# Kernel tuning notes

Measured on AMD Instinct MI355X. Metric: run time of the kernel, lower is better.

## Reference

```python
import jax, jax.numpy as jnp
import numpy as np

H = 128          # hidden_dim
L = 10           # num_iterations
NC = 8000        # check nodes
NV = 16000       # var nodes
E = 60000        # edges per direction
INPUT_SCALE = 0.1
LN_EPS = 1e-6


def _glorot(key, shape):
    fan_in, fan_out = shape[0], shape[-1]
    lim = np.sqrt(6.0 / (fan_in + fan_out))
    return jax.random.uniform(key, shape, jnp.float32, -lim, lim)


def _ln(x, g, b):
    m = jnp.mean(x, axis=-1, keepdims=True)
    v = jnp.var(x, axis=-1, keepdims=True)
    return g * (x - m) / jnp.sqrt(v + LN_EPS) + b


def _gru(x, h, W, U, b):
    # Keras GRUCell, reset_after=True; gate order: z (update), r (reset), h (candidate)
    xa = x @ W + b[0]            # [N, 3H]
    ha = h @ U + b[1]            # [N, 3H]
    z = jax.nn.sigmoid(xa[:, :H] + ha[:, :H])
    r = jax.nn.sigmoid(xa[:, H:2 * H] + ha[:, H:2 * H])
    hh = jnp.tanh(xa[:, 2 * H:] + r * ha[:, 2 * H:])
    return z * h + (1.0 - z) * hh


def setup_inputs() -> dict:
    key = jax.random.key(0)
    ks = jax.random.split(key, 24)
    d = {
        'check_feats': jax.random.normal(ks[0], (NC, 1), jnp.float32),
        'var_feats': jax.random.normal(ks[1], (NV, 1), jnp.float32),
        'c2v_src': jax.random.randint(ks[2], (E,), 0, NC, jnp.int32),
        'c2v_tgt': jax.random.randint(ks[3], (E,), 0, NV, jnp.int32),
        'v2c_src': jax.random.randint(ks[4], (E,), 0, NV, jnp.int32),
        'v2c_tgt': jax.random.randint(ks[5], (E,), 0, NC, jnp.int32),
        # input transforms (Dense 1->H) + LayerNorm params
        'Wc_in': _glorot(ks[6], (1, H)), 'bc_in': jnp.zeros((H,), jnp.float32),
        'Wv_in': _glorot(ks[7], (1, H)), 'bv_in': jnp.zeros((H,), jnp.float32),
        'gc_ln': jnp.ones((H,), jnp.float32), 'bc_ln': jnp.zeros((H,), jnp.float32),
        'gv_ln': jnp.ones((H,), jnp.float32), 'bv_ln': jnp.zeros((H,), jnp.float32),
        # SimpleConv message Dense(2H->H) per receiving node set
        'Wmsg_c': _glorot(ks[8], (2 * H, H)), 'bmsg_c': jnp.zeros((H,), jnp.float32),
        'Wmsg_v': _glorot(ks[9], (2 * H, H)), 'bmsg_v': jnp.zeros((H,), jnp.float32),
        # NextStateFromConcat Dense(2H->H)
        'Wns_c': _glorot(ks[10], (2 * H, H)), 'bns_c': jnp.zeros((H,), jnp.float32),
        'Wns_v': _glorot(ks[11], (2 * H, H)), 'bns_v': jnp.zeros((H,), jnp.float32),
        # GRU cells: kernel [H,3H], recurrent [H,3H], bias [2,3H]
        'Wg_c': _glorot(ks[12], (H, 3 * H)), 'Ug_c': _glorot(ks[13], (H, 3 * H)),
        'bg_c': jnp.zeros((2, 3 * H), jnp.float32),
        'Wg_v': _glorot(ks[14], (H, 3 * H)), 'Ug_v': _glorot(ks[15], (H, 3 * H)),
        'bg_v': jnp.zeros((2, 3 * H), jnp.float32),
        # final predictor Dense(H->1), bias = logit(p_error)
        'Wf': _glorot(ks[16], (H, 1)),
        'bf': jnp.full((1,), np.log((4.0 / NV) / (1 - 4.0 / NV)), jnp.float32),
    }
    return d


def reference(check_feats, var_feats, c2v_src, c2v_tgt, v2c_src, v2c_tgt,
              Wc_in, bc_in, Wv_in, bv_in, gc_ln, bc_ln, gv_ln, bv_ln,
              Wmsg_c, bmsg_c, Wmsg_v, bmsg_v, Wns_c, bns_c, Wns_v, bns_v,
              Wg_c, Ug_c, bg_c, Wg_v, Ug_v, bg_v, Wf, bf):
    hc = _ln((INPUT_SCALE * check_feats) @ Wc_in + bc_in, gc_ln, bc_ln)  # [NC,H]
    hv = _ln((INPUT_SCALE * var_feats) @ Wv_in + bv_in, gv_ln, bv_ln)    # [NV,H]
    for _ in range(L):
        # v_to_c SimpleConv: concat(sender var state, receiver check state) -> Dense+ELU -> scatter-sum
        m_vc = jax.nn.elu(jnp.concatenate([hv[v2c_src], hc[v2c_tgt]], axis=-1) @ Wmsg_c + bmsg_c)
        agg_c = jax.ops.segment_sum(m_vc, v2c_tgt, num_segments=NC)
        # c_to_v SimpleConv
        m_cv = jax.nn.elu(jnp.concatenate([hc[c2v_src], hv[c2v_tgt]], axis=-1) @ Wmsg_v + bmsg_v)
        agg_v = jnp.asarray(jax.ops.segment_sum(m_cv, c2v_tgt, num_segments=NV))
        # NextStateFromConcat: Dense(concat(old_state, pooled)) + ELU
        upd_c = jax.nn.elu(jnp.concatenate([hc, agg_c], axis=-1) @ Wns_c + bns_c)
        upd_v = jax.nn.elu(jnp.concatenate([hv, agg_v], axis=-1) @ Wns_v + bns_v)
        # GRU state update (update info is the input, prev state is the hidden state)
        hc = _gru(upd_c, hc, Wg_c, Ug_c, bg_c)
        hv = _gru(upd_v, hv, Wg_v, Ug_v, bg_v)
    # dropout is identity at inference; final Dense(H->1), squeeze
    return (hv @ Wf + bf)[:, 0]
```

## Files before the change

kernel.cpp:

```cpp
#include <hip/hip_runtime.h>
#include <hip/hip_bf16.h>
#include <math.h>

#define Hdim 128
#define NCn  8000
#define NVn  16000
#define NE   60000
#define LITERS 10
#define NCB16 500
#define NVB16 1000
#define NCB32 250
#define NVB32 500
#define PREPB 1280
#define INITB 6000
#define ZEROB 188
#define FILLB 235

typedef __attribute__((ext_vector_type(8))) short s8v;
typedef __attribute__((ext_vector_type(4))) float f4v;

__device__ __forceinline__ float fexp(float x) { return __expf(x); }
__device__ __forceinline__ float elu_f(float x) { return x > 0.0f ? x : (fexp(x) - 1.0f); }
__device__ __forceinline__ float sigm_f(float x) {
    return __builtin_amdgcn_rcpf(1.0f + fexp(-x));
}
__device__ __forceinline__ float tanh_f(float x) {
    return 1.0f - 2.0f * __builtin_amdgcn_rcpf(1.0f + fexp(2.0f * x));
}
__device__ __forceinline__ unsigned short f2b(float x) {
    __hip_bfloat16 h = __float2bfloat16(x); return *(unsigned short*)&h;
}
__device__ __forceinline__ float b2f(unsigned short u) {
    __hip_bfloat16 h; *(unsigned short*)&h = u; return __bfloat162float(h);
}

__global__ void prep_init(const float* __restrict__ Wmsg_c, const float* __restrict__ Wmsg_v,
                          const float* __restrict__ Wns_c,  const float* __restrict__ Wns_v,
                          const float* __restrict__ Wg_c, const float* __restrict__ Ug_c,
                          const float* __restrict__ Wg_v, const float* __restrict__ Ug_v,
                          unsigned short* __restrict__ Fmsg_c, unsigned short* __restrict__ Fmsg_v,
                          unsigned short* __restrict__ Fns_c,  unsigned short* __restrict__ Fns_v,
                          unsigned short* __restrict__ Fcat_c, unsigned short* __restrict__ Fcat_v,
                          const float* __restrict__ cf, const float* __restrict__ vf,
                          const float* __restrict__ Wc, const float* __restrict__ bc,
                          const float* __restrict__ Wv, const float* __restrict__ bv,
                          const float* __restrict__ gc, const float* __restrict__ bcl,
                          const float* __restrict__ gv, const float* __restrict__ bvl,
                          float* __restrict__ hc, float* __restrict__ hv,
                          int* __restrict__ cnts) {
    if (blockIdx.x >= PREPB + INITB) {
        int i = (blockIdx.x - PREPB - INITB) * 256 + threadIdx.x;
        if (i < 48000) cnts[i] = 0;
        return;
    }
    if (blockIdx.x < PREPB) {
        int idx = blockIdx.x * 256 + threadIdx.x;
        const int S1 = 4 * 32768;
        const int S2 = S1 + 2 * 98304;
        if (idx < S1) {
            int seg = idx >> 15, t = idx & 32767;
            const float* W = (seg == 0) ? Wmsg_c : (seg == 1) ? Wmsg_v : (seg == 2) ? Wns_c : Wns_v;
            unsigned short* outw = (seg == 0) ? Fmsg_c : (seg == 1) ? Fmsg_v : (seg == 2) ? Fns_c : Fns_v;
            int j = t & 7, lane = (t >> 3) & 63, t2 = t >> 9;
            int f = t2 & 7, kt = t2 >> 3;
            int n = f * 16 + (lane & 15), k = kt * 32 + (lane >> 4) * 8 + j;
            outw[t] = f2b(W[(size_t)k * 128 + n]);
        } else if (idx < S2) {
            int q = idx - S1;
            int seg = q / 98304, t = q - seg * 98304;
            const float* Wg = seg ? Wg_v : Wg_c;
            const float* Ug = seg ? Ug_v : Ug_c;
            unsigned short* outw = seg ? Fcat_v : Fcat_c;
            int j = t & 7, lane = (t >> 3) & 63, t2 = t >> 9;
            int f = t2 % 24, kt = t2 / 24;
            int n = f * 16 + (lane & 15), k = kt * 32 + (lane >> 4) * 8 + j;
            outw[t] = f2b((k < 128) ? Ug[(size_t)k * 384 + n] : Wg[(size_t)(k - 128) * 384 + n]);
        }
        return;
    }
    int node = (blockIdx.x - PREPB) * 4 + (threadIdx.x >> 6);
    int lane = threadIdx.x & 63;
    const float *Win, *bin, *g, *bl;
    float f;
    float* outp;
    if (node < NCn) {
        f = cf[node]; Win = Wc; bin = bc; g = gc; bl = bcl;
        outp = hc + (size_t)node * Hdim;
    } else {
        int n2 = node - NCn;
        f = vf[n2]; Win = Wv; bin = bv; g = gv; bl = bvl;
        outp = hv + (size_t)n2 * Hdim;
    }
    f *= 0.1f;
    float x0 = f * Win[lane] + bin[lane];
    float x1 = f * Win[lane + 64] + bin[lane + 64];
    float s = x0 + x1;
    float sq = x0 * x0 + x1 * x1;
    #pragma unroll
    for (int off = 32; off > 0; off >>= 1) {
        s += __shfl_xor(s, off);
        sq += __shfl_xor(sq, off);
    }
    float m = s * (1.0f / 128.0f);
    float v = sq * (1.0f / 128.0f) - m * m;
    float inv = 1.0f / sqrtf(v + 1e-6f);
    outp[lane]      = g[lane]      * (x0 - m) * inv + bl[lane];
    outp[lane + 64] = g[lane + 64] * (x1 - m) * inv + bl[lane + 64];
}

__global__ void hist_kernel(const int* __restrict__ tgt_c, const int* __restrict__ tgt_v,
                            int* __restrict__ cnt_c, int* __restrict__ cnt_v) {
    int e = blockIdx.x * blockDim.x + threadIdx.x;
    if (e >= NE) return;
    atomicAdd(&cnt_c[tgt_c[e]], 1);
    atomicAdd(&cnt_v[tgt_v[e]], 1);
}
__launch_bounds__(1024)
__global__ void scan2_kernel(const int* __restrict__ cnt_c, int* __restrict__ rp_c,
                             const int* __restrict__ cnt_v, int* __restrict__ rp_v) {
    const int* cnt = blockIdx.x ? cnt_v : cnt_c;
    int* rowptr = blockIdx.x ? rp_v : rp_c;
    const int n = blockIdx.x ? NVn : NCn;
    __shared__ int part[1024];
    int t = threadIdx.x;
    int chunk = (n + 1023) >> 10;
    int base = t * chunk;
    int s = 0;
    for (int i = 0; i < chunk; i++) { int idx = base + i; if (idx < n) s += cnt[idx]; }
    part[t] = s;
    __syncthreads();
    for (int off = 1; off < 1024; off <<= 1) {
        int u = (t >= off) ? part[t - off] : 0;
        __syncthreads();
        part[t] += u;
        __syncthreads();
    }
    int run = part[t] - s;
    for (int i = 0; i < chunk; i++) {
        int idx = base + i;
        if (idx < n) { rowptr[idx] = run; run += cnt[idx]; }
    }
    if (t == 0) rowptr[n] = part[1023];
}

__launch_bounds__(256)
__global__ void fill_pq(const int* __restrict__ tgt_c, const int* __restrict__ tgt_v,
                        const int* __restrict__ src_c, const int* __restrict__ src_v,
                        const int* __restrict__ rp_c, const int* __restrict__ rp_v,
                        int* __restrict__ fill_c, int* __restrict__ fill_v,
                        int* __restrict__ srcs_c, int* __restrict__ srcs_v,
                        const float* __restrict__ hc, const float* __restrict__ hv,
                        const unsigned short* __restrict__ Fmsg_c, const unsigned short* __restrict__ Fmsg_v,
                        const float* __restrict__ bmsg_c, const float* __restrict__ bmsg_v,
                        unsigned short* __restrict__ Pv_w, unsigned short* __restrict__ Qc_w,
                        unsigned short* __restrict__ Pc_w, unsigned short* __restrict__ Qv_w) {
    if (blockIdx.x < FILLB) {
        int e = blockIdx.x * 256 + threadIdx.x;
        if (e >= NE) return;
        int tc = tgt_c[e];
        srcs_c[rp_c[tc] + atomicAdd(&fill_c[tc], 1)] = src_c[e];
        int tv = tgt_v[e];
        srcs_v[rp_v[tv] + atomicAdd(&fill_v[tv], 1)] = src_v[e];
        return;
    }
    __shared__ unsigned short sA[32 * 136];
    const int bid = blockIdx.x - FILLB;
    const int isV = (bid >= NCB32) ? 1 : 0;
    const int blockM = (isV ? (bid - NCB32) : bid) * 32;
    const float* h = isV ? hv : hc;
    const unsigned short* FP = isV ? Fmsg_c : Fmsg_v;
    const unsigned short* FQ = isV ? Fmsg_v : Fmsg_c;
    const float* bq = isV ? bmsg_v : bmsg_c;
    unsigned short* Pw = isV ? Pv_w : Pc_w;
    unsigned short* Qw = isV ? Qv_w : Qc_w;

    const int tid = threadIdx.x;
    const int lane = tid & 63, wave = tid >> 6;
    const int quad = lane >> 4, l16 = lane & 15;
    {
        int rr = tid >> 3, cc = tid & 7;
        const float* hrow = &h[(size_t)(blockM + rr) * Hdim + cc * 16];
        f4v x0 = *(const f4v*)hrow;
        f4v x1 = *(const f4v*)(hrow + 4);
        f4v x2 = *(const f4v*)(hrow + 8);
        f4v x3 = *(const f4v*)(hrow + 12);
        s8v w0, w1;
        #pragma unroll
        for (int i = 0; i < 4; i++) {
            w0[i] = (short)f2b(x0[i]); w0[i + 4] = (short)f2b(x1[i]);
            w1[i] = (short)f2b(x2[i]); w1[i + 4] = (short)f2b(x3[i]);
        }
        *(s8v*)&sA[rr * 136 + cc * 16]     = w0;
        *(s8v*)&sA[rr * 136 + cc * 16 + 8] = w1;
    }
    __syncthreads();

    f4v accP[2][2], accQ[2][2];
    #pragma unroll
    for (int mt = 0; mt < 2; mt++)
        #pragma unroll
        for (int u = 0; u < 2; u++) { accP[mt][u] = (f4v){0.f,0.f,0.f,0.f}; accQ[mt][u] = (f4v){0.f,0.f,0.f,0.f}; }

    #pragma unroll
    for (int kt = 0; kt < 4; kt++) {
        s8v a0 = *(const s8v*)&sA[l16 * 136 + kt * 32 + quad * 8];
        s8v a1 = *(const s8v*)&sA[(16 + l16) * 136 + kt * 32 + quad * 8];
        #pragma unroll
        for (int u = 0; u < 2; u++) {
            int ct = wave * 2 + u;
            s8v bp = *(const s8v*)&FP[((size_t)(kt * 8 + ct) * 64 + lane) * 8];
            s8v bqv = *(const s8v*)&FQ[((size_t)((kt + 4) * 8 + ct) * 64 + lane) * 8];
            accP[0][u] = __builtin_amdgcn_mfma_f32_16x16x32_bf16(a0, bp, accP[0][u], 0, 0, 0);
            accP[1][u] = __builtin_amdgcn_mfma_f32_16x16x32_bf16(a1, bp, accP[1][u], 0, 0, 0);
            accQ[0][u] = __builtin_amdgcn_mfma_f32_16x16x32_bf16(a0, bqv, accQ[0][u], 0, 0, 0);
            accQ[1][u] = __builtin_amdgcn_mfma_f32_16x16x32_bf16(a1, bqv, accQ[1][u], 0, 0, 0);
        }
    }
    #pragma unroll
    for (int u = 0; u < 2; u++) {
        int col = (wave * 2 + u) * 16 + l16;
        float qbias = bq[col];
        #pragma unroll
        for (int mt = 0; mt < 2; mt++)
            #pragma unroll
            for (int reg = 0; reg < 4; reg++) {
                int row = blockM + mt * 16 + quad * 4 + reg;
                Pw[(size_t)row * Hdim + col] = f2b(accP[mt][u][reg]);
                Qw[(size_t)row * Hdim + col] = f2b(accQ[mt][u][reg] + qbias);
            }
    }
}

__launch_bounds__(256)
__global__ void node_fused(float* __restrict__ hc, float* __restrict__ hv,
                           const int* __restrict__ rp_c, const int* __restrict__ rp_v,
                           const int* __restrict__ srcs_c, const int* __restrict__ srcs_v,
                           const unsigned short* __restrict__ Pv_r, const unsigned short* __restrict__ Qc_r,
                           const unsigned short* __restrict__ Pc_r, const unsigned short* __restrict__ Qv_r,
                           unsigned short* __restrict__ Pv_w, unsigned short* __restrict__ Qc_w,
                           unsigned short* __restrict__ Pc_w, unsigned short* __restrict__ Qv_w,
                           const unsigned short* __restrict__ Fns_c, const float* __restrict__ bns_c,
                           const unsigned short* __restrict__ Fns_v, const float* __restrict__ bns_v,
                           const unsigned short* __restrict__ Fcat_c, const unsigned short* __restrict__ Fcat_v,
                           const float* __restrict__ bg_c, const float* __restrict__ bg_v,
                           const unsigned short* __restrict__ Fmsg_c, const unsigned short* __restrict__ Fmsg_v,
                           const float* __restrict__ bmsg_c, const float* __restrict__ bmsg_v,
                           const float* __restrict__ Wf, const float* __restrict__ bf,
                           float* __restrict__ out, int do_pq, int vOnly) {
    __shared__ unsigned short sA[16 * 264];
    __shared__ unsigned short sU[16 * 136];
    __shared__ float sHf[16 * 128];
    __shared__ float sRed[64];
    const int bid = blockIdx.x;
    const int isV = vOnly ? 1 : ((bid >= NCB16) ? 1 : 0);
    const int blockM = (vOnly ? bid : (isV ? (bid - NCB16) : bid)) * 16;
    float* h = isV ? hv : hc;
    const int* rp = isV ? rp_v : rp_c;
    const int* srcs = isV ? srcs_v : srcs_c;
    const unsigned short* Pr = isV ? Pc_r : Pv_r;
    const unsigned short* Qr = isV ? Qv_r : Qc_r;
    const unsigned short* Fns = isV ? Fns_v : Fns_c;
    const float* bns = isV ? bns_v : bns_c;
    const unsigned short* Fcat = isV ? Fcat_v : Fcat_c;
    const float* bg = isV ? bg_v : bg_c;
    const unsigned short* FP = isV ? Fmsg_c : Fmsg_v;
    const unsigned short* FQ = isV ? Fmsg_v : Fmsg_c;
    const float* bq = isV ? bmsg_v : bmsg_c;
    unsigned short* Pw = isV ? Pv_w : Pc_w;
    unsigned short* Qw = isV ? Qv_w : Qc_w;

    const int tid = threadIdx.x;
    const int lane = tid & 63, wave = tid >> 6;
    const int quad = lane >> 4, l16 = lane & 15;
    const int r = tid >> 4, ch = tid & 15;
    const int node = blockM + r;

    {
        s8v q8 = *(const s8v*)&Qr[(size_t)node * Hdim + ch * 8];
        const float* hrow = &h[(size_t)node * Hdim + ch * 8];
        f4v h0 = *(const f4v*)hrow;
        f4v h1 = *(const f4v*)(hrow + 4);
        int j = rp[node];
        const int e0 = rp[node + 1];

        s8v hw;
        #pragma unroll
        for (int i = 0; i < 4; i++) { hw[i] = (short)f2b(h0[i]); hw[i + 4] = (short)f2b(h1[i]); }
        *(s8v*)&sA[r * 264 + ch * 8] = hw;
        *(f4v*)&sHf[r * 128 + ch * 8]     = h0;
        *(f4v*)&sHf[r * 128 + ch * 8 + 4] = h1;

        float qf[8], acc[8];
        #pragma unroll
        for (int i = 0; i < 8; i++) { qf[i] = b2f((unsigned short)q8[i]); acc[i] = 0.0f; }

        for (; j + 8 <= e0; j += 8) {
            s8v p[8];
            #pragma unroll
            for (int b = 0; b < 8; b++)
                p[b] = *(const s8v*)&Pr[(size_t)srcs[j + b] * Hdim + ch * 8];
            #pragma unroll
            for (int b = 0; b < 8; b++)
                #pragma unroll
                for (int i = 0; i < 8; i++) acc[i] += elu_f(b2f((unsigned short)p[b][i]) + qf[i]);
        }
        if (j + 4 <= e0) {
            s8v p[4];
            #pragma unroll
            for (int b = 0; b < 4; b++)
                p[b] = *(const s8v*)&Pr[(size_t)srcs[j + b] * Hdim + ch * 8];
            #pragma unroll
            for (int b = 0; b < 4; b++)
                #pragma unroll
                for (int i = 0; i < 8; i++) acc[i] += elu_f(b2f((unsigned short)p[b][i]) + qf[i]);
            j += 4;
        }
        if (j + 2 <= e0) {
            s8v p0 = *(const s8v*)&Pr[(size_t)srcs[j] * Hdim + ch * 8];
            s8v p1 = *(const s8v*)&Pr[(size_t)srcs[j + 1] * Hdim + ch * 8];
            #pragma unroll
            for (int i = 0; i < 8; i++) acc[i] += elu_f(b2f((unsigned short)p0[i]) + qf[i]);
            #pragma unroll
            for (int i = 0; i < 8; i++) acc[i] += elu_f(b2f((unsigned short)p1[i]) + qf[i]);
            j += 2;
        }
        if (j < e0) {
            s8v p0 = *(const s8v*)&Pr[(size_t)srcs[j] * Hdim + ch * 8];
            #pragma unroll
            for (int i = 0; i < 8; i++) acc[i] += elu_f(b2f((unsigned short)p0[i]) + qf[i]);
        }
        s8v w;
        #pragma unroll
        for (int i = 0; i < 8; i++) w[i] = (short)f2b(acc[i]);
        *(s8v*)&sA[r * 264 + 128 + ch * 8] = w;
    }
    __syncthreads();

    f4v accA[2];
    accA[0] = (f4v){0.f,0.f,0.f,0.f};
    accA[1] = (f4v){0.f,0.f,0.f,0.f};
    #pragma unroll
    for (int kt = 0; kt < 8; kt++) {
        s8v a = *(const s8v*)&sA[l16 * 264 + kt * 32 + quad * 8];
        #pragma unroll
        for (int u = 0; u < 2; u++) {
            s8v b = *(const s8v*)&Fns[((size_t)(kt * 8 + wave * 2 + u) * 64 + lane) * 8];
            accA[u] = __builtin_amdgcn_mfma_f32_16x16x32_bf16(a, b, accA[u], 0, 0, 0);
        }
    }
    #pragma unroll
    for (int u = 0; u < 2; u++) {
        int col = (wave * 2 + u) * 16 + l16;
        float bb = bns[col];
        #pragma unroll
        for (int reg = 0; reg < 4; reg++)
            sU[(quad * 4 + reg) * 136 + col] = f2b(elu_f(accA[u][reg] + bb));
    }
    __syncthreads();

    float hnv[2][4];
    #pragma unroll
    for (int u = 0; u < 2; u++) {
        const int j = wave * 2 + u;
        f4v sZ = (f4v){0.f,0.f,0.f,0.f};
        f4v sR = (f4v){0.f,0.f,0.f,0.f};
        f4v sH1 = (f4v){0.f,0.f,0.f,0.f};
        f4v sH2 = (f4v){0.f,0.f,0.f,0.f};
        #pragma unroll
        for (int kt = 0; kt < 8; kt++) {
            s8v a = (kt < 4)
                ? *(const s8v*)&sA[l16 * 264 + kt * 32 + quad * 8]
                : *(const s8v*)&sU[l16 * 136 + (kt - 4) * 32 + quad * 8];
            s8v bz = *(const s8v*)&Fcat[((size_t)(kt * 24 + j) * 64 + lane) * 8];
            s8v br = *(const s8v*)&Fcat[((size_t)(kt * 24 + 8 + j) * 64 + lane) * 8];
            s8v bh = *(const s8v*)&Fcat[((size_t)(kt * 24 + 16 + j) * 64 + lane) * 8];
            sZ = __builtin_amdgcn_mfma_f32_16x16x32_bf16(a, bz, sZ, 0, 0, 0);
            sR = __builtin_amdgcn_mfma_f32_16x16x32_bf16(a, br, sR, 0, 0, 0);
            if (kt < 4)
                sH1 = __builtin_amdgcn_mfma_f32_16x16x32_bf16(a, bh, sH1, 0, 0, 0);
            else
                sH2 = __builtin_amdgcn_mfma_f32_16x16x32_bf16(a, bh, sH2, 0, 0, 0);
        }
        const int t = j * 16 + l16;
        float bz2 = bg[t]       + bg[384 + t];
        float br2 = bg[128 + t] + bg[512 + t];
        float b0h = bg[256 + t];
        float b1h = bg[640 + t];
        #pragma unroll
        for (int reg = 0; reg < 4; reg++) {
            int rloc = quad * 4 + reg;
            float z = sigm_f(sZ[reg] + sH1[reg] * 0.0f + bz2 + 0.0f);
            z = sigm_f(sZ[reg] + bz2);
            float rr = sigm_f(sR[reg] + br2);
            float hh = tanh_f((sH2[reg] + b0h) + rr * (sH1[reg] + b1h));
            float hold = sHf[rloc * 128 + t];
            float hn = z * hold + (1.0f - z) * hh;
            if (do_pq) h[(size_t)(blockM + rloc) * Hdim + t] = hn;
            hnv[u][reg] = hn;
        }
    }

    if (!do_pq) {
        float wf0 = Wf[(wave * 2 + 0) * 16 + l16];
        float wf1 = Wf[(wave * 2 + 1) * 16 + l16];
        float part[4];
        #pragma unroll
        for (int reg = 0; reg < 4; reg++)
            part[reg] = hnv[0][reg] * wf0 + hnv[1][reg] * wf1;
        #pragma unroll
        for (int off = 1; off < 16; off <<= 1) {
            #pragma unroll
            for (int reg = 0; reg < 4; reg++)
                part[reg] += __shfl_xor(part[reg], off);
        }
        if (l16 == 0) {
            #pragma unroll
            for (int reg = 0; reg < 4; reg++)
                sRed[wave * 16 + quad * 4 + reg] = part[reg];
        }
        __syncthreads();
        if (tid < 16)
            out[blockM + tid] = sRed[tid] + sRed[16 + tid] + sRed[32 + tid] + sRed[48 + tid] + bf[0];
        return;
    }

    __syncthreads();
    #pragma unroll
    for (int u = 0; u < 2; u++) {
        int col = (wave * 2 + u) * 16 + l16;
        #pragma unroll
        for (int reg = 0; reg < 4; reg++)
            sA[(quad * 4 + reg) * 264 + col] = f2b(hnv[u][reg]);
    }
    __syncthreads();

    f4v accP[2], accQ[2];
    accP[0] = (f4v){0.f,0.f,0.f,0.f}; accP[1] = (f4v){0.f,0.f,0.f,0.f};
    accQ[0] = (f4v){0.f,0.f,0.f,0.f}; accQ[1] = (f4v){0.f,0.f,0.f,0.f};
    #pragma unroll
    for (int kt = 0; kt < 4; kt++) {
        s8v a = *(const s8v*)&sA[l16 * 264 + kt * 32 + quad * 8];
        #pragma unroll
        for (int u = 0; u < 2; u++) {
            int ct = wave * 2 + u;
            s8v bp = *(const s8v*)&FP[((size_t)(kt * 8 + ct) * 64 + lane) * 8];
            s8v bqv = *(const s8v*)&FQ[((size_t)((kt + 4) * 8 + ct) * 64 + lane) * 8];
            accP[u] = __builtin_amdgcn_mfma_f32_16x16x32_bf16(a, bp, accP[u], 0, 0, 0);
            accQ[u] = __builtin_amdgcn_mfma_f32_16x16x32_bf16(a, bqv, accQ[u], 0, 0, 0);
        }
    }
    #pragma unroll
    for (int u = 0; u < 2; u++) {
        int col = (wave * 2 + u) * 16 + l16;
        float qbias = bq[col];
        #pragma unroll
        for (int reg = 0; reg < 4; reg++) {
            int row = blockM + quad * 4 + reg;
            Pw[(size_t)row * Hdim + col] = f2b(accP[u][reg]);
            Qw[(size_t)row * Hdim + col] = f2b(accQ[u][reg] + qbias);
        }
    }
}

extern "C" void kernel_launch(void* const* d_in, const int* in_sizes, int n_in,
                              void* d_out, int out_size, void* d_ws, size_t ws_size,
                              hipStream_t stream) {
    const float* cf      = (const float*)d_in[0];
    const float* vf      = (const float*)d_in[1];
    const int*   c2v_src = (const int*)d_in[2];
    const int*   c2v_tgt = (const int*)d_in[3];
    const int*   v2c_src = (const int*)d_in[4];
    const int*   v2c_tgt = (const int*)d_in[5];
    const float* Wc_in   = (const float*)d_in[6];
    const float* bc_in   = (const float*)d_in[7];
    const float* Wv_in   = (const float*)d_in[8];
    const float* bv_in   = (const float*)d_in[9];
    const float* gc_ln   = (const float*)d_in[10];
    const float* bc_ln   = (const float*)d_in[11];
    const float* gv_ln   = (const float*)d_in[12];
    const float* bv_ln   = (const float*)d_in[13];
    const float* Wmsg_c  = (const float*)d_in[14];
    const float* bmsg_c  = (const float*)d_in[15];
    const float* Wmsg_v  = (const float*)d_in[16];
    const float* bmsg_v  = (const float*)d_in[17];
    const float* Wns_c   = (const float*)d_in[18];
    const float* bns_c   = (const float*)d_in[19];
    const float* Wns_v   = (const float*)d_in[20];
    const float* bns_v   = (const float*)d_in[21];
    const float* Wg_c    = (const float*)d_in[22];
    const float* Ug_c    = (const float*)d_in[23];
    const float* bg_c    = (const float*)d_in[24];
    const float* Wg_v    = (const float*)d_in[25];
    const float* Ug_v    = (const float*)d_in[26];
    const float* bg_v    = (const float*)d_in[27];
    const float* Wf      = (const float*)d_in[28];
    const float* bf      = (const float*)d_in[29];
    float* out = (float*)d_out;

    char* p = (char*)d_ws;
    #define CARVE(name, type, count) type* name = (type*)p; p += (((size_t)(count) * sizeof(type)) + 255) & ~(size_t)255;
    CARVE(hc,     float, NCn * Hdim)
    CARVE(hv,     float, NVn * Hdim)
    CARVE(Pv0,    unsigned short, NVn * Hdim)
    CARVE(Qc0,    unsigned short, NCn * Hdim)
    CARVE(Pc0,    unsigned short, NCn * Hdim)
    CARVE(Qv0,    unsigned short, NVn * Hdim)
    CARVE(Pv1,    unsigned short, NVn * Hdim)
    CARVE(Qc1,    unsigned short, NCn * Hdim)
    CARVE(Pc1,    unsigned short, NCn * Hdim)
    CARVE(Qv1,    unsigned short, NVn * Hdim)
    CARVE(Fmsg_c, unsigned short, 32768)
    CARVE(Fmsg_v, unsigned short, 32768)
    CARVE(Fns_c,  unsigned short, 32768)
    CARVE(Fns_v,  unsigned short, 32768)
    CARVE(Fcat_c, unsigned short, 98304)
    CARVE(Fcat_v, unsigned short, 98304)
    CARVE(rp_c,  int, NCn + 8)
    CARVE(rp_v,  int, NVn + 8)
    CARVE(srcs_c, int, NE)
    CARVE(srcs_v, int, NE)
    CARVE(cnts,  int, 48000)
    #undef CARVE
    int* cnt_c  = cnts;
    int* cnt_v  = cnts + NCn;
    int* fill_c = cnts + NCn + NVn;
    int* fill_v = cnts + 2 * NCn + NVn;

    prep_init<<<PREPB + INITB + ZEROB, 256, 0, stream>>>(
        Wmsg_c, Wmsg_v, Wns_c, Wns_v, Wg_c, Ug_c, Wg_v, Ug_v,
        Fmsg_c, Fmsg_v, Fns_c, Fns_v, Fcat_c, Fcat_v,
        cf, vf, Wc_in, bc_in, Wv_in, bv_in, gc_ln, bc_ln, gv_ln, bv_ln, hc, hv, cnts);
    hist_kernel<<<(NE + 255) / 256, 256, 0, stream>>>(v2c_tgt, c2v_tgt, cnt_c, cnt_v);
    scan2_kernel<<<2, 1024, 0, stream>>>(cnt_c, rp_c, cnt_v, rp_v);
    fill_pq<<<FILLB + NCB32 + NVB32, 256, 0, stream>>>(
        v2c_tgt, c2v_tgt, v2c_src, c2v_src, rp_c, rp_v, fill_c, fill_v, srcs_c, srcs_v,
        hc, hv, Fmsg_c, Fmsg_v, bmsg_c, bmsg_v, Pv0, Qc0, Pc0, Qv0);

    unsigned short* Pv_[2] = {Pv0, Pv1};
    unsigned short* Qc_[2] = {Qc0, Qc1};
    unsigned short* Pc_[2] = {Pc0, Pc1};
    unsigned short* Qv_[2] = {Qv0, Qv1};

    for (int it = 0; it < LITERS; it++) {
        int rd = it & 1, wr = rd ^ 1;
        int last = (it == LITERS - 1);
        node_fused<<<last ? NVB16 : (NCB16 + NVB16), 256, 0, stream>>>(
            hc, hv, rp_c, rp_v, srcs_c, srcs_v,
            Pv_[rd], Qc_[rd], Pc_[rd], Qv_[rd],
            Pv_[wr], Qc_[wr], Pc_[wr], Qv_[wr],
            Fns_c, bns_c, Fns_v, bns_v,
            Fcat_c, Fcat_v, bg_c, bg_v,
            Fmsg_c, Fmsg_v, bmsg_c, bmsg_v,
            Wf, bf, out, last ? 0 : 1, last ? 1 : 0);
    }
}
```

Measured before the change: 499.7 us.

## Fold histogram into prep kernel, use wave-shuffle scan, pad shared h tile

The separate histogram kernel is merged into the prep/init launch, and the zeroing of count buffers moves to a hipMemsetAsync issued beforehand. The 1024-thread scan drops its log-step shared-memory loop with many barriers in favour of a wave-level shuffle scan plus a small per-wave sum pass. The shared float tile of old hidden states gets a row stride of 132 instead of 128 to reduce LDS bank conflicts, and a redundant sigmoid evaluation in the GRU epilogue is removed. These cut launch overhead and setup latency, but add a memset call whose cost may offset part of the saving.

After: 501.9 us. No clear change (+0.4%).

```diff
diff --git a/kernel.cpp b/kernel.cpp
--- a/kernel.cpp
+++ b/kernel.cpp
@@ -13,7 +13,7 @@
 #define NVB32 500
 #define PREPB 1280
 #define INITB 6000
-#define ZEROB 188
+#define HISTB 235
 #define FILLB 235
 
 typedef __attribute__((ext_vector_type(8))) short s8v;
@@ -47,10 +47,13 @@
                           const float* __restrict__ gc, const float* __restrict__ bcl,
                           const float* __restrict__ gv, const float* __restrict__ bvl,
                           float* __restrict__ hc, float* __restrict__ hv,
-                          int* __restrict__ cnts) {
+                          const int* __restrict__ tgt_c, const int* __restrict__ tgt_v,
+                          int* __restrict__ cnt_c, int* __restrict__ cnt_v) {
     if (blockIdx.x >= PREPB + INITB) {
-        int i = (blockIdx.x - PREPB - INITB) * 256 + threadIdx.x;
-        if (i < 48000) cnts[i] = 0;
+        int e = (blockIdx.x - PREPB - INITB) * 256 + threadIdx.x;
+        if (e >= NE) return;
+        atomicAdd(&cnt_c[tgt_c[e]], 1);
+        atomicAdd(&cnt_v[tgt_v[e]], 1);
         return;
     }
     if (blockIdx.x < PREPB) {
@@ -108,39 +111,44 @@
     outp[lane + 64] = g[lane + 64] * (x1 - m) * inv + bl[lane + 64];
 }
 
-__global__ void hist_kernel(const int* __restrict__ tgt_c, const int* __restrict__ tgt_v,
-                            int* __restrict__ cnt_c, int* __restrict__ cnt_v) {
-    int e = blockIdx.x * blockDim.x + threadIdx.x;
-    if (e >= NE) return;
-    atomicAdd(&cnt_c[tgt_c[e]], 1);
-    atomicAdd(&cnt_v[tgt_v[e]], 1);
-}
 __launch_bounds__(1024)
 __global__ void scan2_kernel(const int* __restrict__ cnt_c, int* __restrict__ rp_c,
                              const int* __restrict__ cnt_v, int* __restrict__ rp_v) {
     const int* cnt = blockIdx.x ? cnt_v : cnt_c;
     int* rowptr = blockIdx.x ? rp_v : rp_c;
     const int n = blockIdx.x ? NVn : NCn;
-    __shared__ int part[1024];
+    __shared__ int wsum[16];
     int t = threadIdx.x;
+    int lane = t & 63, wid = t >> 6;
     int chunk = (n + 1023) >> 10;
     int base = t * chunk;
     int s = 0;
     for (int i = 0; i < chunk; i++) { int idx = base + i; if (idx < n) s += cnt[idx]; }
-    part[t] = s;
-    __syncthreads();
-    for (int off = 1; off < 1024; off <<= 1) {
-        int u = (t >= off) ? part[t - off] : 0;
-        __syncthreads();
-        part[t] += u;
-        __syncthreads();
-    }
-    int run = part[t] - s;
+    int sc = s;
+    #pragma unroll
+    for (int off = 1; off < 64; off <<= 1) {
+        int u = __shfl_up(sc, off);
+        if (lane >= off) sc += u;
+    }
+    if (lane == 63) wsum[wid] = sc;
+    __syncthreads();
+    if (wid == 0 && lane < 16) {
+        int w = wsum[lane];
+        int wscan = w;
+        #pragma unroll
+        for (int off = 1; off < 16; off <<= 1) {
+            int u = __shfl_up(wscan, off);
+            if (lane >= off) wscan += u;
+        }
+        wsum[lane] = wscan - w;
+    }
+    __syncthreads();
+    int run = wsum[wid] + sc - s;
     for (int i = 0; i < chunk; i++) {
         int idx = base + i;
         if (idx < n) { rowptr[idx] = run; run += cnt[idx]; }
     }
-    if (t == 0) rowptr[n] = part[1023];
+    if (t == 1023) rowptr[n] = wsum[15] + sc;
 }
 
 __launch_bounds__(256)
@@ -249,7 +257,7 @@
                            float* __restrict__ out, int do_pq, int vOnly) {
     __shared__ unsigned short sA[16 * 264];
     __shared__ unsigned short sU[16 * 136];
-    __shared__ float sHf[16 * 128];
+    __shared__ float sHf[16 * 132];
     __shared__ float sRed[64];
     const int bid = blockIdx.x;
     const int isV = vOnly ? 1 : ((bid >= NCB16) ? 1 : 0);
@@ -287,8 +295,8 @@
         #pragma unroll
         for (int i = 0; i < 4; i++) { hw[i] = (short)f2b(h0[i]); hw[i + 4] = (short)f2b(h1[i]); }
         *(s8v*)&sA[r * 264 + ch * 8] = hw;
-        *(f4v*)&sHf[r * 128 + ch * 8]     = h0;
-        *(f4v*)&sHf[r * 128 + ch * 8 + 4] = h1;
+        *(f4v*)&sHf[r * 132 + ch * 8]     = h0;
+        *(f4v*)&sHf[r * 132 + ch * 8 + 4] = h1;
 
         float qf[8], acc[8];
         #pragma unroll
@@ -389,11 +397,10 @@
         #pragma unroll
         for (int reg = 0; reg < 4; reg++) {
             int rloc = quad * 4 + reg;
-            float z = sigm_f(sZ[reg] + sH1[reg] * 0.0f + bz2 + 0.0f);
-            z = sigm_f(sZ[reg] + bz2);
+            float z = sigm_f(sZ[reg] + bz2);
             float rr = sigm_f(sR[reg] + br2);
             float hh = tanh_f((sH2[reg] + b0h) + rr * (sH1[reg] + b1h));
-            float hold = sHf[rloc * 128 + t];
+            float hold = sHf[rloc * 132 + t];
             float hn = z * hold + (1.0f - z) * hh;
             if (do_pq) h[(size_t)(blockM + rloc) * Hdim + t] = hn;
             hnv[u][reg] = hn;
@@ -526,11 +533,12 @@
     int* fill_c = cnts + NCn + NVn;
     int* fill_v = cnts + 2 * NCn + NVn;
 
-    prep_init<<<PREPB + INITB + ZEROB, 256, 0, stream>>>(
+    hipMemsetAsync(cnts, 0, 48000 * sizeof(int), stream);
+    prep_init<<<PREPB + INITB + HISTB, 256, 0, stream>>>(
         Wmsg_c, Wmsg_v, Wns_c, Wns_v, Wg_c, Ug_c, Wg_v, Ug_v,
         Fmsg_c, Fmsg_v, Fns_c, Fns_v, Fcat_c, Fcat_v,
-        cf, vf, Wc_in, bc_in, Wv_in, bv_in, gc_ln, bc_ln, gv_ln, bv_ln, hc, hv, cnts);
-    hist_kernel<<<(NE + 255) / 256, 256, 0, stream>>>(v2c_tgt, c2v_tgt, cnt_c, cnt_v);
+        cf, vf, Wc_in, bc_in, Wv_in, bv_in, gc_ln, bc_ln, gv_ln, bv_ln, hc, hv,
+        v2c_tgt, c2v_tgt, cnt_c, cnt_v);
     scan2_kernel<<<2, 1024, 0, stream>>>(cnt_c, rp_c, cnt_v, rp_v);
     fill_pq<<<FILLB + NCB32 + NVB32, 256, 0, stream>>>(
         v2c_tgt, c2v_tgt, v2c_src, c2v_src, rp_c, rp_v, fill_c, fill_v, srcs_c, srcs_v,
```
